# Performance work log

Measured on AMD Instinct MI355X. Metric: run time of the kernel, lower is better.

Reference implementation:

```python
import jax, jax.numpy as jnp
import numpy as np

B, C, N = 16, 128, 2048  # batch, channels (SA_Layer(128)), num points


def setup_inputs() -> dict:
    key = jax.random.key(0)
    ks = jax.random.split(key, 6)
    x = jax.random.normal(ks[0], (B, C, N), jnp.float32)
    wq = jax.random.normal(ks[1], (C // 4, C), jnp.float32) * 0.05  # shared q/k 1x1 conv, no bias
    wv = jax.random.normal(ks[2], (C, C), jnp.float32) * 0.05
    bv = jax.random.normal(ks[3], (C,), jnp.float32) * 0.05
    wt = jax.random.normal(ks[4], (C, C), jnp.float32) * 0.05
    bt = jax.random.normal(ks[5], (C,), jnp.float32) * 0.05
    gamma = jnp.ones((C,), jnp.float32)   # BatchNorm1d weight
    beta = jnp.zeros((C,), jnp.float32)   # BatchNorm1d bias
    bn_mean = jnp.zeros((C,), jnp.float32)  # running mean (eval mode)
    bn_var = jnp.ones((C,), jnp.float32)    # running var (eval mode)
    return dict(x=x, wq=wq, wv=wv, bv=bv, wt=wt, bt=bt,
                gamma=gamma, beta=beta, bn_mean=bn_mean, bn_var=bn_var)


def reference(x, wq, wv, bv, wt, bt, gamma, beta, bn_mean, bn_var):
    EPS = 1e-9
    BN_EPS = 1e-5
    # q_conv and k_conv share weights (tied in __init__)
    x_q = jnp.einsum('dc,bcn->bnd', wq, x)               # [B, N, C/4]
    x_k = jnp.einsum('dc,bcn->bdn', wq, x)               # [B, C/4, N]
    energy = jnp.einsum('bnd,bdm->bnm', x_q, x_k)        # [B, N, N]
    attn = jax.nn.softmax(energy, axis=-1)
    # offset-attention renormalization: divide by column sum
    attn = attn / (EPS + attn.sum(axis=1, keepdims=True))
    x_v = jnp.einsum('dc,bcn->bdn', wv, x) + bv[None, :, None]   # [B, C, N]
    x_r = jnp.einsum('bdn,bnm->bdm', x_v, attn)                  # [B, C, N]
    t = jnp.einsum('dc,bcn->bdn', wt, x - x_r) + bt[None, :, None]
    # BatchNorm1d (eval mode) + ReLU
    t = (t - bn_mean[None, :, None]) * jax.lax.rsqrt(bn_var + BN_EPS)[None, :, None]
    t = t * gamma[None, :, None] + beta[None, :, None]
    return x + jax.nn.relu(t)
```

## Files before the change

### kernel.cpp

```cpp
#include <hip/hip_runtime.h>
#include <hip/hip_bf16.h>
#include <math.h>

#define BB 16
#define CC 128
#define NN 2048
#define CQ 32

typedef __attribute__((ext_vector_type(8))) short bf16x8;
typedef __attribute__((ext_vector_type(4))) float f32x4;
typedef __attribute__((ext_vector_type(16))) float f32x16;

__device__ __forceinline__ ushort f2b(float f) {
    __hip_bfloat16 h = __float2bfloat16(f);
    return *reinterpret_cast<ushort*>(&h);
}
__device__ __forceinline__ float b2f(ushort u) {
    union { unsigned u; float f; } v; v.u = ((unsigned)u) << 16;
    return v.f;
}
__device__ __forceinline__ bf16x8 as_b8(uint4 u) {
    union { uint4 u; bf16x8 b; } v; v.u = u; return v.b;
}
__device__ __forceinline__ bf16x8 as_b8_2(uint2 a, uint2 b) {
    return as_b8(make_uint4(a.x, a.y, b.x, b.y));
}
__device__ __forceinline__ float fexp2(float x) {
    return __builtin_amdgcn_exp2f(x);
}

#define OFF_VB  524288
#define OFF_RSI 4718592

#define QSCALE 1.2011224087864498f

__global__ __launch_bounds__(256) void k_proj(const float* __restrict__ x,
        const float* __restrict__ wq, const float* __restrict__ wv,
        const float* __restrict__ bv, ushort* __restrict__ Qt, ushort* __restrict__ Vb) {
    __shared__ ushort Wl[160][136];
    __shared__ ushort Xs[64][136];
    int bid = (blockIdx.x & 7) * 64 + (blockIdx.x >> 3);
    int b  = bid >> 5;
    int n0 = (bid & 31) << 6;
    int tid = threadIdx.x;
    #pragma unroll
    for (int k = 0; k < 20; ++k) {
        int idx = k * 256 + tid;
        int r = idx >> 5, c4 = (idx & 31) << 2;
        const float* srcw = (r < 32) ? (wq + r * 128 + c4) : (wv + (r - 32) * 128 + c4);
        float4 w4 = *(const float4*)srcw;
        float s = (r < 32) ? QSCALE : 1.0f;
        *(ushort4*)&Wl[r][c4] = make_ushort4(f2b(w4.x * s), f2b(w4.y * s),
                                             f2b(w4.z * s), f2b(w4.w * s));
    }
    const float* xb = x + (size_t)b * CC * NN;
    for (int idx = tid; idx < 2048; idx += 256) {
        int c = idx >> 4, n4 = (idx & 15) << 2;
        float4 xv = *(const float4*)&xb[c * NN + n0 + n4];
        Xs[n4][c]     = f2b(xv.x);
        Xs[n4 + 1][c] = f2b(xv.y);
        Xs[n4 + 2][c] = f2b(xv.z);
        Xs[n4 + 3][c] = f2b(xv.w);
    }
    __syncthreads();
    int w = tid >> 6, l = tid & 63, lr = l & 15, lg = l >> 4;
    f32x4 zero = {0.f, 0.f, 0.f, 0.f};
    int nn = n0 + w * 16 + lr;
    for (int dt = 0; dt < 10; ++dt) {
        f32x4 acc = zero;
        #pragma unroll
        for (int k = 0; k < 4; ++k) {
            bf16x8 a  = *(const bf16x8*)&Wl[dt * 16 + lr][k * 32 + lg * 8];
            bf16x8 bx = *(const bf16x8*)&Xs[w * 16 + lr][k * 32 + lg * 8];
            acc = __builtin_amdgcn_mfma_f32_16x16x32_bf16(a, bx, acc, 0, 0, 0);
        }
        if (dt < 2) {
            ushort4 p = make_ushort4(f2b(acc[0]), f2b(acc[1]), f2b(acc[2]), f2b(acc[3]));
            *(ushort4*)&Qt[(size_t)(b * NN + nn) * CQ + dt * 16 + lg * 4] = p;
        } else {
            #pragma unroll
            for (int i = 0; i < 4; ++i) {
                int vd = (dt - 2) * 16 + lg * 4 + i;
                Vb[(size_t)(b * CC + vd) * NN + nn] = f2b(acc[i] + bv[vd]);
            }
        }
    }
}

__global__ __launch_bounds__(512) void k_rowstats(const ushort* __restrict__ Qt,
        float* __restrict__ RSI) {
    __shared__ ushort Qm[128][36];
    __shared__ float Sred[2][64];
    int bid = (blockIdx.x & 7) * 64 + (blockIdx.x >> 3);
    int b  = bid >> 5;
    int n0 = (bid & 31) << 6;
    int tid = threadIdx.x;
    int w = tid >> 6, l = tid & 63, lr = l & 15, lg = l >> 4;
    int wn = w & 3, wm = w >> 2;
    const ushort* Qtb = Qt + (size_t)b * NN * CQ;
    bf16x8 aq = *(const bf16x8*)&Qtb[(size_t)(n0 + wn * 16 + lr) * CQ + lg * 8];
    int sr = tid >> 2, sc = (tid & 3) * 8;
    uint4 q0 = *(const uint4*)&Qtb[(size_t)sr * CQ + sc];
    float S[4] = {0.f, 0.f, 0.f, 0.f};
    f32x4 zero = {0.f, 0.f, 0.f, 0.f};
    for (int t = 0; t < 16; ++t) {
        __syncthreads();
        *(uint4*)&Qm[sr][sc] = q0;
        __syncthreads();
        if (t < 15)
            q0 = *(const uint4*)&Qtb[(size_t)((t + 1) * 128 + sr) * CQ + sc];
        #pragma unroll
        for (int mi = 0; mi < 4; ++mi) {
            bf16x8 bq = *(const bf16x8*)&Qm[(wm * 4 + mi) * 16 + lr][lg * 8];
            f32x4 e = __builtin_amdgcn_mfma_f32_16x16x32_bf16(aq, bq, zero, 0, 0, 0);
            S[0] += fexp2(e[0]); S[1] += fexp2(e[1]);
            S[2] += fexp2(e[2]); S[3] += fexp2(e[3]);
        }
    }
    #pragma unroll
    for (int d = 1; d < 16; d <<= 1) {
        #pragma unroll
        for (int i = 0; i < 4; ++i) S[i] += __shfl_xor(S[i], d);
    }
    if (lr == 0) {
        #pragma unroll
        for (int i = 0; i < 4; ++i) Sred[wm][wn * 16 + lg * 4 + i] = S[i];
    }
    __syncthreads();
    if (tid < 64)
        RSI[b * NN + n0 + tid] = 1.f / (Sred[0][tid] + Sred[1][tid]);
}

__global__ __launch_bounds__(768, 3) void k_attn_pv(const ushort* __restrict__ Qt,
        const ushort* __restrict__ Vb, const float* __restrict__ RSI,
        const float* __restrict__ x, const float* __restrict__ wt,
        const float* __restrict__ bt, const float* __restrict__ gamma,
        const float* __restrict__ beta, const float* __restrict__ bn_mean,
        const float* __restrict__ bn_var, float* __restrict__ out) {
    __shared__ ushort Vs[2][128][68];
    __shared__ ushort Ws[2][128][68];
    __shared__ ushort wtl[16896];
    __shared__ float csred[4][128];
    __shared__ float csum[128];
    __shared__ float fAl[128], fBl[128];
    int bid = (blockIdx.x & 7) * 32 + (blockIdx.x >> 3);
    int b  = bid >> 4;
    int m0 = (bid & 15) << 7;
    int tid = threadIdx.x;
    int w = tid >> 6, l = tid & 63, lr = l & 15, lg = l >> 4;
    const ushort* Qtb = Qt + (size_t)b * NN * CQ;
    const ushort* Vbb = Vb + (size_t)b * CC * NN;
    const float*  RSb = RSI + (size_t)b * NN;
    const float*  xb  = x   + (size_t)b * CC * NN;
    float*        outb = out + (size_t)b * CC * NN;
    f32x4 zero = {0.f, 0.f, 0.f, 0.f};
    bool producer = (w < 8);

    for (int idx = tid; idx < 4096; idx += 768) {
        int r = idx >> 5, c4 = (idx & 31) << 2;
        float4 w4 = *(const float4*)&wt[r * 128 + c4];
        *(ushort4*)&wtl[r * 132 + c4] =
            make_ushort4(f2b(w4.x), f2b(w4.y), f2b(w4.z), f2b(w4.w));
    }
    if (tid < 128) {
        float A = gamma[tid] * rsqrtf(bn_var[tid] + 1e-5f);
        fAl[tid] = A;
        fBl[tid] = (bt[tid] - bn_mean[tid]) * A + beta[tid];
    }

    int wn = w & 3, mh = w >> 2;
    bf16x8 bm[4];
    float cs[4] = {0.f, 0.f, 0.f, 0.f};
    int sv = 0, shv = 0;
    const ushort* vsrc = nullptr;
    bf16x8 aq_nx; float4 rsi_nx;
    int cw = w - 8;
    int dh = cw >> 1, mh2 = cw & 1;
    int ar = l & 31, kh = l >> 5;
    f32x16 pacc00, pacc01, pacc10, pacc11;

    if (producer) {
        #pragma unroll
        for (int mi = 0; mi < 4; ++mi)
            bm[mi] = *(const bf16x8*)&Qtb[(size_t)(m0 + (mh * 4 + mi) * 16 + lr) * CQ + lg * 8];
        sv = tid >> 2; shv = (tid & 3) * 16;
        vsrc = Vbb + (size_t)sv * NN + shv;
        {
            uint4 v0 = *(const uint4*)(vsrc);
            uint4 v1 = *(const uint4*)(vsrc + 8);
            ushort* dst = &Vs[0][sv][shv];
            *(uint2*)(dst)      = make_uint2(v0.x, v0.y);
            *(uint2*)(dst + 4)  = make_uint2(v0.z, v0.w);
            *(uint2*)(dst + 8)  = make_uint2(v1.x, v1.y);
            *(uint2*)(dst + 12) = make_uint2(v1.z, v1.w);
        }
        {
            bf16x8 aq0 = *(const bf16x8*)&Qtb[(size_t)(wn * 16 + lr) * CQ + lg * 8];
            float4 r4 = *(const float4*)&RSb[wn * 16 + lg * 4];
            int nb = wn * 16 + lg * 4;
            #pragma unroll
            for (int mi = 0; mi < 4; ++mi) {
                f32x4 e = __builtin_amdgcn_mfma_f32_16x16x32_bf16(aq0, bm[mi], zero, 0, 0, 0);
                float w0 = fexp2(e[0]) * r4.x;
                float w1 = fexp2(e[1]) * r4.y;
                float w2 = fexp2(e[2]) * r4.z;
                float w3 = fexp2(e[3]) * r4.w;
                cs[mi] += w0 + w1 + w2 + w3;
                *(ushort4*)&Ws[0][(mh * 4 + mi) * 16 + lr][nb] =
                    make_ushort4(f2b(w0), f2b(w1), f2b(w2), f2b(w3));
            }
        }
        aq_nx  = *(const bf16x8*)&Qtb[(size_t)(64 + wn * 16 + lr) * CQ + lg * 8];
        rsi_nx = *(const float4*)&RSb[64 + wn * 16 + lg * 4];
    } else {
        #pragma unroll
        for (int r = 0; r < 16; ++r) {
            pacc00[r] = 0.f; pacc01[r] = 0.f; pacc10[r] = 0.f; pacc11[r] = 0.f;
        }
    }
    __syncthreads();
    for (int t = 0; t < 32; ++t) {
        int cur = t & 1;
        if (producer) {
            if (t < 31) {
                int ntn = (t + 1) * 64;
                uint4 v0 = *(const uint4*)(vsrc + ntn);
                uint4 v1 = *(const uint4*)(vsrc + ntn + 8);
                bf16x8 aq = aq_nx;
                float4 r4 = rsi_nx;
                if (t < 30) {
                    int nt2 = (t + 2) * 64;
                    aq_nx  = *(const bf16x8*)&Qtb[(size_t)(nt2 + wn * 16 + lr) * CQ + lg * 8];
                    rsi_nx = *(const float4*)&RSb[nt2 + wn * 16 + lg * 4];
                }
                int nb = wn * 16 + lg * 4;
                #pragma unroll
                for (int mi = 0; mi < 4; ++mi) {
                    f32x4 e = __builtin_amdgcn_mfma_f32_16x16x32_bf16(aq, bm[mi], zero, 0, 0, 0);
                    float w0 = fexp2(e[0]) * r4.x;
                    float w1 = fexp2(e[1]) * r4.y;
                    float w2 = fexp2(e[2]) * r4.z;
                    float w3 = fexp2(e[3]) * r4.w;
                    cs[mi] += w0 + w1 + w2 + w3;
                    *(ushort4*)&Ws[cur ^ 1][(mh * 4 + mi) * 16 + lr][nb] =
                        make_ushort4(f2b(w0), f2b(w1), f2b(w2), f2b(w3));
                }
                ushort* dst = &Vs[cur ^ 1][sv][shv];
                *(uint2*)(dst)      = make_uint2(v0.x, v0.y);
                *(uint2*)(dst + 4)  = make_uint2(v0.z, v0.w);
                *(uint2*)(dst + 8)  = make_uint2(v1.x, v1.y);
                *(uint2*)(dst + 12) = make_uint2(v1.z, v1.w);
            }
        } else {
            __builtin_amdgcn_s_setprio(1);
            #pragma unroll
            for (int kk = 0; kk < 4; ++kk) {
                const ushort* vp0 = &Vs[cur][dh * 64 + ar][kk * 16 + kh * 8];
                const ushort* vp1 = &Vs[cur][dh * 64 + 32 + ar][kk * 16 + kh * 8];
                uint2 a0 = *(const uint2*)vp0; uint2 a1 = *(const uint2*)(vp0 + 4);
                uint2 a2 = *(const uint2*)vp1; uint2 a3 = *(const uint2*)(vp1 + 4);
                bf16x8 va0 = as_b8_2(a0, a1);
                bf16x8 va1 = as_b8_2(a2, a3);
                const ushort* wp0 = &Ws[cur][mh2 * 64 + ar][kk * 16 + kh * 8];
                const ushort* wp1 = &Ws[cur][mh2 * 64 + 32 + ar][kk * 16 + kh * 8];
                uint2 b0 = *(const uint2*)wp0; uint2 b1 = *(const uint2*)(wp0 + 4);
                uint2 c0 = *(const uint2*)wp1; uint2 c1 = *(const uint2*)(wp1 + 4);
                bf16x8 wb0 = as_b8_2(b0, b1);
                bf16x8 wb1 = as_b8_2(c0, c1);
                pacc00 = __builtin_amdgcn_mfma_f32_32x32x16_bf16(va0, wb0, pacc00, 0, 0, 0);
                pacc01 = __builtin_amdgcn_mfma_f32_32x32x16_bf16(va0, wb1, pacc01, 0, 0, 0);
                pacc10 = __builtin_amdgcn_mfma_f32_32x32x16_bf16(va1, wb0, pacc10, 0, 0, 0);
                pacc11 = __builtin_amdgcn_mfma_f32_32x32x16_bf16(va1, wb1, pacc11, 0, 0, 0);
            }
            __builtin_amdgcn_s_setprio(0);
        }
        __syncthreads();
    }
    if (producer) {
        #pragma unroll
        for (int mi = 0; mi < 4; ++mi) {
            cs[mi] += __shfl_xor(cs[mi], 16);
            cs[mi] += __shfl_xor(cs[mi], 32);
        }
        if (lg == 0) {
            #pragma unroll
            for (int mi = 0; mi < 4; ++mi)
                csred[wn][(mh * 4 + mi) * 16 + lr] = cs[mi];
        }
    }
    __syncthreads();
    if (tid < 128) {
        float tot = csred[0][tid] + csred[1][tid] + csred[2][tid] + csred[3][tid];
        csum[tid] = 1.f / (1e-9f + tot);
    }
    __syncthreads();
    ushort* UsP = &Vs[0][0][0];
    if (!producer) {
        float inv0 = csum[mh2 * 64 + ar];
        float inv1 = csum[mh2 * 64 + 32 + ar];
        int mA = m0 + mh2 * 64 + ar;
        int mL = mh2 * 64 + ar;
        #pragma unroll
        for (int g = 0; g < 4; ++g) {
            int db = dh * 64 + 8 * g + 4 * kh;
            ushort4 u00, u01, u10, u11;
            #pragma unroll
            for (int j = 0; j < 4; ++j) {
                int r = 4 * g + j;
                float x00 = xb[(size_t)(db + j) * NN + mA];
                float x01 = xb[(size_t)(db + j) * NN + mA + 32];
                float x10 = xb[(size_t)(db + 32 + j) * NN + mA];
                float x11 = xb[(size_t)(db + 32 + j) * NN + mA + 32];
                ((ushort*)&u00)[j] = f2b(x00 - pacc00[r] * inv0);
                ((ushort*)&u01)[j] = f2b(x01 - pacc01[r] * inv1);
                ((ushort*)&u10)[j] = f2b(x10 - pacc10[r] * inv0);
                ((ushort*)&u11)[j] = f2b(x11 - pacc11[r] * inv1);
            }
            *(ushort4*)&UsP[mL * 132 + db]             = u00;
            *(ushort4*)&UsP[(mL + 32) * 132 + db]      = u01;
            *(ushort4*)&UsP[mL * 132 + db + 32]        = u10;
            *(ushort4*)&UsP[(mL + 32) * 132 + db + 32] = u11;
        }
    }
    __syncthreads();
    for (int tile = w; tile < 16; tile += 12) {
        int rt = tile >> 2, mt = tile & 3;
        f32x16 acc;
        #pragma unroll
        for (int r = 0; r < 16; ++r) acc[r] = 0.f;
        #pragma unroll
        for (int kk = 0; kk < 8; ++kk) {
            const ushort* ap = &wtl[(rt * 32 + ar) * 132 + kk * 16 + kh * 8];
            uint2 a0 = *(const uint2*)ap; uint2 a1 = *(const uint2*)(ap + 4);
            const ushort* bp = &UsP[(mt * 32 + ar) * 132 + kk * 16 + kh * 8];
            uint2 b0 = *(const uint2*)bp; uint2 b1 = *(const uint2*)(bp + 4);
            acc = __builtin_amdgcn_mfma_f32_32x32x16_bf16(
                as_b8_2(a0, a1), as_b8_2(b0, b1), acc, 0, 0, 0);
        }
        int m = m0 + mt * 32 + ar;
        #pragma unroll
        for (int g = 0; g < 4; ++g) {
            #pragma unroll
            for (int j = 0; j < 4; ++j) {
                int r = rt * 32 + j + 8 * g + 4 * kh;
                float t = acc[4 * g + j] * fAl[r] + fBl[r];
                t = fmaxf(t, 0.f);
                outb[(size_t)r * NN + m] = xb[(size_t)r * NN + m] + t;
            }
        }
    }
}

extern "C" void kernel_launch(void* const* d_in, const int* in_sizes, int n_in,
                              void* d_out, int out_size, void* d_ws, size_t ws_size,
                              hipStream_t stream) {
    const float* x       = (const float*)d_in[0];
    const float* wq      = (const float*)d_in[1];
    const float* wv      = (const float*)d_in[2];
    const float* bv      = (const float*)d_in[3];
    const float* wt      = (const float*)d_in[4];
    const float* bt      = (const float*)d_in[5];
    const float* gamma   = (const float*)d_in[6];
    const float* beta    = (const float*)d_in[7];
    const float* bn_mean = (const float*)d_in[8];
    const float* bn_var  = (const float*)d_in[9];
    float* out = (float*)d_out;
    float* ws  = (float*)d_ws;

    ushort* Qt   = (ushort*)ws;
    ushort* Vbp  = (ushort*)(ws + OFF_VB);
    float*  RSI  = ws + OFF_RSI;

    k_proj<<<BB * 32, 256, 0, stream>>>(x, wq, wv, bv, Qt, Vbp);
    k_rowstats<<<BB * 32, 512, 0, stream>>>(Qt, RSI);
    k_attn_pv<<<BB * 16, 768, 0, stream>>>(Qt, Vbp, RSI, x, wt, bt, gamma, beta,
                                           bn_mean, bn_var, out);
}
```

Baseline: 62.50 us.

## Quad-buffer V/W tiles, process two tiles per barrier, read wt from global

The producer/consumer loop now uses four LDS buffers and handles two 64-wide tiles per iteration, so the number of block-wide barriers drops from 32 to 16. The shared bf16 copy of wt is removed to free LDS for the extra buffers; the epilogue GEMM now loads wt as fp32 from global memory and converts it to bf16 in registers. In exchange, the producer no longer prefetches its next tile, and each consumer wave re-reads and re-converts wt from global. LDS use per block also rises, which may reduce how many blocks fit per CU.

```diff
diff --git a/kernel.cpp b/kernel.cpp
--- a/kernel.cpp
+++ b/kernel.cpp
@@ -137,9 +137,8 @@
         const float* __restrict__ bt, const float* __restrict__ gamma,
         const float* __restrict__ beta, const float* __restrict__ bn_mean,
         const float* __restrict__ bn_var, float* __restrict__ out) {
-    __shared__ ushort Vs[2][128][68];
-    __shared__ ushort Ws[2][128][68];
-    __shared__ ushort wtl[16896];
+    __shared__ ushort Vs[4][128][68];
+    __shared__ ushort Ws[4][128][68];
     __shared__ float csred[4][128];
     __shared__ float csum[128];
     __shared__ float fAl[128], fBl[128];
@@ -156,12 +155,6 @@
     f32x4 zero = {0.f, 0.f, 0.f, 0.f};
     bool producer = (w < 8);
 
-    for (int idx = tid; idx < 4096; idx += 768) {
-        int r = idx >> 5, c4 = (idx & 31) << 2;
-        float4 w4 = *(const float4*)&wt[r * 128 + c4];
-        *(ushort4*)&wtl[r * 132 + c4] =
-            make_ushort4(f2b(w4.x), f2b(w4.y), f2b(w4.z), f2b(w4.w));
-    }
     if (tid < 128) {
         float A = gamma[tid] * rsqrtf(bn_var[tid] + 1e-5f);
         fAl[tid] = A;
@@ -173,7 +166,6 @@
     float cs[4] = {0.f, 0.f, 0.f, 0.f};
     int sv = 0, shv = 0;
     const ushort* vsrc = nullptr;
-    bf16x8 aq_nx; float4 rsi_nx;
     int cw = w - 8;
     int dh = cw >> 1, mh2 = cw & 1;
     int ar = l & 31, kh = l >> 5;
@@ -185,93 +177,95 @@
             bm[mi] = *(const bf16x8*)&Qtb[(size_t)(m0 + (mh * 4 + mi) * 16 + lr) * CQ + lg * 8];
         sv = tid >> 2; shv = (tid & 3) * 16;
         vsrc = Vbb + (size_t)sv * NN + shv;
-        {
-            uint4 v0 = *(const uint4*)(vsrc);
-            uint4 v1 = *(const uint4*)(vsrc + 8);
-            ushort* dst = &Vs[0][sv][shv];
-            *(uint2*)(dst)      = make_uint2(v0.x, v0.y);
-            *(uint2*)(dst + 4)  = make_uint2(v0.z, v0.w);
-            *(uint2*)(dst + 8)  = make_uint2(v1.x, v1.y);
-            *(uint2*)(dst + 12) = make_uint2(v1.z, v1.w);
-        }
-        {
-            bf16x8 aq0 = *(const bf16x8*)&Qtb[(size_t)(wn * 16 + lr) * CQ + lg * 8];
-            float4 r4 = *(const float4*)&RSb[wn * 16 + lg * 4];
-            int nb = wn * 16 + lg * 4;
-            #pragma unroll
-            for (int mi = 0; mi < 4; ++mi) {
-                f32x4 e = __builtin_amdgcn_mfma_f32_16x16x32_bf16(aq0, bm[mi], zero, 0, 0, 0);
-                float w0 = fexp2(e[0]) * r4.x;
-                float w1 = fexp2(e[1]) * r4.y;
-                float w2 = fexp2(e[2]) * r4.z;
-                float w3 = fexp2(e[3]) * r4.w;
-                cs[mi] += w0 + w1 + w2 + w3;
-                *(ushort4*)&Ws[0][(mh * 4 + mi) * 16 + lr][nb] =
-                    make_ushort4(f2b(w0), f2b(w1), f2b(w2), f2b(w3));
-            }
-        }
-        aq_nx  = *(const bf16x8*)&Qtb[(size_t)(64 + wn * 16 + lr) * CQ + lg * 8];
-        rsi_nx = *(const float4*)&RSb[64 + wn * 16 + lg * 4];
     } else {
         #pragma unroll
         for (int r = 0; r < 16; ++r) {
             pacc00[r] = 0.f; pacc01[r] = 0.f; pacc10[r] = 0.f; pacc11[r] = 0.f;
         }
     }
-    __syncthreads();
-    for (int t = 0; t < 32; ++t) {
-        int cur = t & 1;
+
+    auto produce2 = [&](int tA) {
+        int tB = tA + 1;
+        int bqA = tA & 3, bqB = tB & 3;
+        int ntA = tA * 64, ntB = tB * 64;
+        uint4 va0 = *(const uint4*)(vsrc + ntA);
+        uint4 va1 = *(const uint4*)(vsrc + ntA + 8);
+        uint4 vb0 = *(const uint4*)(vsrc + ntB);
+        uint4 vb1 = *(const uint4*)(vsrc + ntB + 8);
+        bf16x8 aqA = *(const bf16x8*)&Qtb[(size_t)(ntA + wn * 16 + lr) * CQ + lg * 8];
+        bf16x8 aqB = *(const bf16x8*)&Qtb[(size_t)(ntB + wn * 16 + lr) * CQ + lg * 8];
+        float4 r4A = *(const float4*)&RSb[ntA + wn * 16 + lg * 4];
+        float4 r4B = *(const float4*)&RSb[ntB + wn * 16 + lg * 4];
+        int nb = wn * 16 + lg * 4;
+        #pragma unroll
+        for (int mi = 0; mi < 4; ++mi) {
+            f32x4 e = __builtin_amdgcn_mfma_f32_16x16x32_bf16(aqA, bm[mi], zero, 0, 0, 0);
+            float w0 = fexp2(e[0]) * r4A.x;
+            float w1 = fexp2(e[1]) * r4A.y;
+            float w2 = fexp2(e[2]) * r4A.z;
+            float w3 = fexp2(e[3]) * r4A.w;
+            cs[mi] += w0 + w1 + w2 + w3;
+            *(ushort4*)&Ws[bqA][(mh * 4 + mi) * 16 + lr][nb] =
+                make_ushort4(f2b(w0), f2b(w1), f2b(w2), f2b(w3));
+        }
+        {
+            ushort* dst = &Vs[bqA][sv][shv];
+            *(uint2*)(dst)      = make_uint2(va0.x, va0.y);
+            *(uint2*)(dst + 4)  = make_uint2(va0.z, va0.w);
+            *(uint2*)(dst + 8)  = make_uint2(va1.x, va1.y);
+            *(uint2*)(dst + 12) = make_uint2(va1.z, va1.w);
+        }
+        #pragma unroll
+        for (int mi = 0; mi < 4; ++mi) {
+            f32x4 e = __builtin_amdgcn_mfma_f32_16x16x32_bf16(aqB, bm[mi], zero, 0, 0, 0);
+            float w0 = fexp2(e[0]) * r4B.x;
+            float w1 = fexp2(e[1]) * r4B.y;
+            float w2 = fexp2(e[2]) * r4B.z;
+            float w3 = fexp2(e[3]) * r4B.w;
+            cs[mi] += w0 + w1 + w2 + w3;
+            *(ushort4*)&Ws[bqB][(mh * 4 + mi) * 16 + lr][nb] =
+                make_ushort4(f2b(w0), f2b(w1), f2b(w2), f2b(w3));
+        }
+        {
+            ushort* dst = &Vs[bqB][sv][shv];
+            *(uint2*)(dst)      = make_uint2(vb0.x, vb0.y);
+            *(uint2*)(dst + 4)  = make_uint2(vb0.z, vb0.w);
+            *(uint2*)(dst + 8)  = make_uint2(vb1.x, vb1.y);
+            *(uint2*)(dst + 12) = make_uint2(vb1.z, vb1.w);
+        }
+    };
+    auto consume = [&](int u) {
+        int bq = u & 3;
+        #pragma unroll
+        for (int kk = 0; kk < 4; ++kk) {
+            const ushort* vp0 = &Vs[bq][dh * 64 + ar][kk * 16 + kh * 8];
+            const ushort* vp1 = &Vs[bq][dh * 64 + 32 + ar][kk * 16 + kh * 8];
+            uint2 a0 = *(const uint2*)vp0; uint2 a1 = *(const uint2*)(vp0 + 4);
+            uint2 a2 = *(const uint2*)vp1; uint2 a3 = *(const uint2*)(vp1 + 4);
+            bf16x8 va0 = as_b8_2(a0, a1);
+            bf16x8 va1 = as_b8_2(a2, a3);
+            const ushort* wp0 = &Ws[bq][mh2 * 64 + ar][kk * 16 + kh * 8];
+            const ushort* wp1 = &Ws[bq][mh2 * 64 + 32 + ar][kk * 16 + kh * 8];
+            uint2 b0 = *(const uint2*)wp0; uint2 b1 = *(const uint2*)(wp0 + 4);
+            uint2 c0 = *(const uint2*)wp1; uint2 c1 = *(const uint2*)(wp1 + 4);
+            bf16x8 wb0 = as_b8_2(b0, b1);
+            bf16x8 wb1 = as_b8_2(c0, c1);
+            pacc00 = __builtin_amdgcn_mfma_f32_32x32x16_bf16(va0, wb0, pacc00, 0, 0, 0);
+            pacc01 = __builtin_amdgcn_mfma_f32_32x32x16_bf16(va0, wb1, pacc01, 0, 0, 0);
+            pacc10 = __builtin_amdgcn_mfma_f32_32x32x16_bf16(va1, wb0, pacc10, 0, 0, 0);
+            pacc11 = __builtin_amdgcn_mfma_f32_32x32x16_bf16(va1, wb1, pacc11, 0, 0, 0);
+        }
+    };
+
+    if (producer) produce2(0);
+    __syncthreads();
+    for (int p = 0; p < 16; ++p) {
         if (producer) {
-            if (t < 31) {
-                int ntn = (t + 1) * 64;
-                uint4 v0 = *(const uint4*)(vsrc + ntn);
-                uint4 v1 = *(const uint4*)(vsrc + ntn + 8);
-                bf16x8 aq = aq_nx;
-                float4 r4 = rsi_nx;
-                if (t < 30) {
-                    int nt2 = (t + 2) * 64;
-                    aq_nx  = *(const bf16x8*)&Qtb[(size_t)(nt2 + wn * 16 + lr) * CQ + lg * 8];
-                    rsi_nx = *(const float4*)&RSb[nt2 + wn * 16 + lg * 4];
-                }
-                int nb = wn * 16 + lg * 4;
-                #pragma unroll
-                for (int mi = 0; mi < 4; ++mi) {
-                    f32x4 e = __builtin_amdgcn_mfma_f32_16x16x32_bf16(aq, bm[mi], zero, 0, 0, 0);
-                    float w0 = fexp2(e[0]) * r4.x;
-                    float w1 = fexp2(e[1]) * r4.y;
-                    float w2 = fexp2(e[2]) * r4.z;
-                    float w3 = fexp2(e[3]) * r4.w;
-                    cs[mi] += w0 + w1 + w2 + w3;
-                    *(ushort4*)&Ws[cur ^ 1][(mh * 4 + mi) * 16 + lr][nb] =
-                        make_ushort4(f2b(w0), f2b(w1), f2b(w2), f2b(w3));
-                }
-                ushort* dst = &Vs[cur ^ 1][sv][shv];
-                *(uint2*)(dst)      = make_uint2(v0.x, v0.y);
-                *(uint2*)(dst + 4)  = make_uint2(v0.z, v0.w);
-                *(uint2*)(dst + 8)  = make_uint2(v1.x, v1.y);
-                *(uint2*)(dst + 12) = make_uint2(v1.z, v1.w);
-            }
+            if (p < 15) produce2(2 * p + 2);
         } else {
             __builtin_amdgcn_s_setprio(1);
-            #pragma unroll
-            for (int kk = 0; kk < 4; ++kk) {
-                const ushort* vp0 = &Vs[cur][dh * 64 + ar][kk * 16 + kh * 8];
-                const ushort* vp1 = &Vs[cur][dh * 64 + 32 + ar][kk * 16 + kh * 8];
-                uint2 a0 = *(const uint2*)vp0; uint2 a1 = *(const uint2*)(vp0 + 4);
-                uint2 a2 = *(const uint2*)vp1; uint2 a3 = *(const uint2*)(vp1 + 4);
-                bf16x8 va0 = as_b8_2(a0, a1);
-                bf16x8 va1 = as_b8_2(a2, a3);
-                const ushort* wp0 = &Ws[cur][mh2 * 64 + ar][kk * 16 + kh * 8];
-                const ushort* wp1 = &Ws[cur][mh2 * 64 + 32 + ar][kk * 16 + kh * 8];
-                uint2 b0 = *(const uint2*)wp0; uint2 b1 = *(const uint2*)(wp0 + 4);
-                uint2 c0 = *(const uint2*)wp1; uint2 c1 = *(const uint2*)(wp1 + 4);
-                bf16x8 wb0 = as_b8_2(b0, b1);
-                bf16x8 wb1 = as_b8_2(c0, c1);
-                pacc00 = __builtin_amdgcn_mfma_f32_32x32x16_bf16(va0, wb0, pacc00, 0, 0, 0);
-                pacc01 = __builtin_amdgcn_mfma_f32_32x32x16_bf16(va0, wb1, pacc01, 0, 0, 0);
-                pacc10 = __builtin_amdgcn_mfma_f32_32x32x16_bf16(va1, wb0, pacc10, 0, 0, 0);
-                pacc11 = __builtin_amdgcn_mfma_f32_32x32x16_bf16(va1, wb1, pacc11, 0, 0, 0);
-            }
+            consume(2 * p);
+            consume(2 * p + 1);
             __builtin_amdgcn_s_setprio(0);
         }
         __syncthreads();
@@ -330,12 +324,18 @@
         for (int r = 0; r < 16; ++r) acc[r] = 0.f;
         #pragma unroll
         for (int kk = 0; kk < 8; ++kk) {
-            const ushort* ap = &wtl[(rt * 32 + ar) * 132 + kk * 16 + kh * 8];
-            uint2 a0 = *(const uint2*)ap; uint2 a1 = *(const uint2*)(ap + 4);
+            const float* ap = &wt[(rt * 32 + ar) * 128 + kk * 16 + kh * 8];
+            float4 wa = *(const float4*)ap;
+            float4 wb4 = *(const float4*)(ap + 4);
+            union { ushort u[8]; bf16x8 v; } af;
+            af.u[0] = f2b(wa.x);  af.u[1] = f2b(wa.y);
+            af.u[2] = f2b(wa.z);  af.u[3] = f2b(wa.w);
+            af.u[4] = f2b(wb4.x); af.u[5] = f2b(wb4.y);
+            af.u[6] = f2b(wb4.z); af.u[7] = f2b(wb4.w);
             const ushort* bp = &UsP[(mt * 32 + ar) * 132 + kk * 16 + kh * 8];
             uint2 b0 = *(const uint2*)bp; uint2 b1 = *(const uint2*)(bp + 4);
             acc = __builtin_amdgcn_mfma_f32_32x32x16_bf16(
-                as_b8_2(a0, a1), as_b8_2(b0, b1), acc, 0, 0, 0);
+                af.v, as_b8_2(b0, b1), acc, 0, 0, 0);
         }
         int m = m0 + mt * 32 + ar;
         #pragma unroll
```

Result: slower. 68.75 us (+10.0%).

## Switch attention-value product to FP8 e4m3 MFMA with scaled weights

Applied to the files above, without the earlier changes.

Stores the V projection and the normalized attention weights as FP8 e4m3 instead of bf16, and runs the PV product with 32x32x16 fp8 MFMA. Row-sum inverses are scaled by 256 so the weights sit in FP8's usable range, and the column-sum epsilon is rescaled to match. This halves the LDS footprint, LDS read traffic and V global reads in the main attention loop. The cost is reduced precision on the attention output, which may exceed the tolerance.

```diff
diff --git a/kernel.cpp b/kernel.cpp
--- a/kernel.cpp
+++ b/kernel.cpp
@@ -1,5 +1,6 @@
 #include <hip/hip_runtime.h>
 #include <hip/hip_bf16.h>
+#include <hip/hip_fp8.h>
 #include <math.h>
 
 #define BB 16
@@ -10,6 +11,7 @@
 typedef __attribute__((ext_vector_type(8))) short bf16x8;
 typedef __attribute__((ext_vector_type(4))) float f32x4;
 typedef __attribute__((ext_vector_type(16))) float f32x16;
+typedef unsigned char uchar;
 
 __device__ __forceinline__ ushort f2b(float f) {
     __hip_bfloat16 h = __float2bfloat16(f);
@@ -19,6 +21,10 @@
     union { unsigned u; float f; } v; v.u = ((unsigned)u) << 16;
     return v.f;
 }
+__device__ __forceinline__ uchar f2q(float f) {
+    __hip_fp8_e4m3 q(f);
+    return *reinterpret_cast<uchar*>(&q);
+}
 __device__ __forceinline__ bf16x8 as_b8(uint4 u) {
     union { uint4 u; bf16x8 b; } v; v.u = u; return v.b;
 }
@@ -28,6 +34,7 @@
 __device__ __forceinline__ float fexp2(float x) {
     return __builtin_amdgcn_exp2f(x);
 }
+union U2L { uint2 u; long l; };
 
 #define OFF_VB  524288
 #define OFF_RSI 4718592
@@ -36,7 +43,7 @@
 
 __global__ __launch_bounds__(256) void k_proj(const float* __restrict__ x,
         const float* __restrict__ wq, const float* __restrict__ wv,
-        const float* __restrict__ bv, ushort* __restrict__ Qt, ushort* __restrict__ Vb) {
+        const float* __restrict__ bv, ushort* __restrict__ Qt, uchar* __restrict__ Vb) {
     __shared__ ushort Wl[160][136];
     __shared__ ushort Xs[64][136];
     int bid = (blockIdx.x & 7) * 64 + (blockIdx.x >> 3);
@@ -81,7 +88,7 @@
             #pragma unroll
             for (int i = 0; i < 4; ++i) {
                 int vd = (dt - 2) * 16 + lg * 4 + i;
-                Vb[(size_t)(b * CC + vd) * NN + nn] = f2b(acc[i] + bv[vd]);
+                Vb[(size_t)(b * CC + vd) * NN + nn] = f2q(acc[i] + bv[vd]);
             }
         }
     }
@@ -128,17 +135,16 @@
     }
     __syncthreads();
     if (tid < 64)
-        RSI[b * NN + n0 + tid] = 1.f / (Sred[0][tid] + Sred[1][tid]);
+        RSI[b * NN + n0 + tid] = 256.f / (Sred[0][tid] + Sred[1][tid]);
 }
 
 __global__ __launch_bounds__(768, 3) void k_attn_pv(const ushort* __restrict__ Qt,
-        const ushort* __restrict__ Vb, const float* __restrict__ RSI,
+        const uchar* __restrict__ Vb, const float* __restrict__ RSI,
         const float* __restrict__ x, const float* __restrict__ wt,
         const float* __restrict__ bt, const float* __restrict__ gamma,
         const float* __restrict__ beta, const float* __restrict__ bn_mean,
         const float* __restrict__ bn_var, float* __restrict__ out) {
-    __shared__ ushort Vs[2][128][68];
-    __shared__ ushort Ws[2][128][68];
+    __shared__ uchar SMp[2][2][128][72];
     __shared__ ushort wtl[16896];
     __shared__ float csred[4][128];
     __shared__ float csum[128];
@@ -149,7 +155,7 @@
     int tid = threadIdx.x;
     int w = tid >> 6, l = tid & 63, lr = l & 15, lg = l >> 4;
     const ushort* Qtb = Qt + (size_t)b * NN * CQ;
-    const ushort* Vbb = Vb + (size_t)b * CC * NN;
+    const uchar*  Vbb = Vb + (size_t)b * CC * NN;
     const float*  RSb = RSI + (size_t)b * NN;
     const float*  xb  = x   + (size_t)b * CC * NN;
     float*        outb = out + (size_t)b * CC * NN;
@@ -172,7 +178,7 @@
     bf16x8 bm[4];
     float cs[4] = {0.f, 0.f, 0.f, 0.f};
     int sv = 0, shv = 0;
-    const ushort* vsrc = nullptr;
+    const uchar* vsrc = nullptr;
     bf16x8 aq_nx; float4 rsi_nx;
     int cw = w - 8;
     int dh = cw >> 1, mh2 = cw & 1;
@@ -187,12 +193,9 @@
         vsrc = Vbb + (size_t)sv * NN + shv;
         {
             uint4 v0 = *(const uint4*)(vsrc);
-            uint4 v1 = *(const uint4*)(vsrc + 8);
-            ushort* dst = &Vs[0][sv][shv];
-            *(uint2*)(dst)      = make_uint2(v0.x, v0.y);
-            *(uint2*)(dst + 4)  = make_uint2(v0.z, v0.w);
-            *(uint2*)(dst + 8)  = make_uint2(v1.x, v1.y);
-            *(uint2*)(dst + 12) = make_uint2(v1.z, v1.w);
+            uchar* dst = &SMp[0][0][sv][shv];
+            *(uint2*)(dst)     = make_uint2(v0.x, v0.y);
+            *(uint2*)(dst + 8) = make_uint2(v0.z, v0.w);
         }
         {
             bf16x8 aq0 = *(const bf16x8*)&Qtb[(size_t)(wn * 16 + lr) * CQ + lg * 8];
@@ -206,8 +209,10 @@
                 float w2 = fexp2(e[2]) * r4.z;
                 float w3 = fexp2(e[3]) * r4.w;
                 cs[mi] += w0 + w1 + w2 + w3;
-                *(ushort4*)&Ws[0][(mh * 4 + mi) * 16 + lr][nb] =
-                    make_ushort4(f2b(w0), f2b(w1), f2b(w2), f2b(w3));
+                union { uchar b[4]; uint u; } pw;
+                pw.b[0] = f2q(w0); pw.b[1] = f2q(w1);
+                pw.b[2] = f2q(w2); pw.b[3] = f2q(w3);
+                *(uint*)&SMp[1][0][(mh * 4 + mi) * 16 + lr][nb] = pw.u;
             }
         }
         aq_nx  = *(const bf16x8*)&Qtb[(size_t)(64 + wn * 16 + lr) * CQ + lg * 8];
@@ -225,7 +230,6 @@
             if (t < 31) {
                 int ntn = (t + 1) * 64;
                 uint4 v0 = *(const uint4*)(vsrc + ntn);
-                uint4 v1 = *(const uint4*)(vsrc + ntn + 8);
                 bf16x8 aq = aq_nx;
                 float4 r4 = rsi_nx;
                 if (t < 30) {
@@ -242,35 +246,29 @@
                     float w2 = fexp2(e[2]) * r4.z;
                     float w3 = fexp2(e[3]) * r4.w;
                     cs[mi] += w0 + w1 + w2 + w3;
-                    *(ushort4*)&Ws[cur ^ 1][(mh * 4 + mi) * 16 + lr][nb] =
-                        make_ushort4(f2b(w0), f2b(w1), f2b(w2), f2b(w3));
+                    union { uchar b[4]; uint u; } pw;
+                    pw.b[0] = f2q(w0); pw.b[1] = f2q(w1);
+                    pw.b[2] = f2q(w2); pw.b[3] = f2q(w3);
+                    *(uint*)&SMp[1][cur ^ 1][(mh * 4 + mi) * 16 + lr][nb] = pw.u;
                 }
-                ushort* dst = &Vs[cur ^ 1][sv][shv];
-                *(uint2*)(dst)      = make_uint2(v0.x, v0.y);
-                *(uint2*)(dst + 4)  = make_uint2(v0.z, v0.w);
-                *(uint2*)(dst + 8)  = make_uint2(v1.x, v1.y);
-                *(uint2*)(dst + 12) = make_uint2(v1.z, v1.w);
+                uchar* dst = &SMp[0][cur ^ 1][sv][shv];
+                *(uint2*)(dst)     = make_uint2(v0.x, v0.y);
+                *(uint2*)(dst + 8) = make_uint2(v0.z, v0.w);
             }
         } else {
             __builtin_amdgcn_s_setprio(1);
             #pragma unroll
             for (int kk = 0; kk < 4; ++kk) {
-                const ushort* vp0 = &Vs[cur][dh * 64 + ar][kk * 16 + kh * 8];
-                const ushort* vp1 = &Vs[cur][dh * 64 + 32 + ar][kk * 16 + kh * 8];
-                uint2 a0 = *(const uint2*)vp0; uint2 a1 = *(const uint2*)(vp0 + 4);
-                uint2 a2 = *(const uint2*)vp1; uint2 a3 = *(const uint2*)(vp1 + 4);
-                bf16x8 va0 = as_b8_2(a0, a1);
-                bf16x8 va1 = as_b8_2(a2, a3);
-                const ushort* wp0 = &Ws[cur][mh2 * 64 + ar][kk * 16 + kh * 8];
-                const ushort* wp1 = &Ws[cur][mh2 * 64 + 32 + ar][kk * 16 + kh * 8];
-                uint2 b0 = *(const uint2*)wp0; uint2 b1 = *(const uint2*)(wp0 + 4);
-                uint2 c0 = *(const uint2*)wp1; uint2 c1 = *(const uint2*)(wp1 + 4);
-                bf16x8 wb0 = as_b8_2(b0, b1);
-                bf16x8 wb1 = as_b8_2(c0, c1);
-                pacc00 = __builtin_amdgcn_mfma_f32_32x32x16_bf16(va0, wb0, pacc00, 0, 0, 0);
-                pacc01 = __builtin_amdgcn_mfma_f32_32x32x16_bf16(va0, wb1, pacc01, 0, 0, 0);
-                pacc10 = __builtin_amdgcn_mfma_f32_32x32x16_bf16(va1, wb0, pacc10, 0, 0, 0);
-                pacc11 = __builtin_amdgcn_mfma_f32_32x32x16_bf16(va1, wb1, pacc11, 0, 0, 0);
+                int cb = kk * 16 + kh * 8;
+                U2L va0, va1, wb0, wb1;
+                va0.u = *(const uint2*)&SMp[0][cur][dh * 64 + ar][cb];
+                va1.u = *(const uint2*)&SMp[0][cur][dh * 64 + 32 + ar][cb];
+                wb0.u = *(const uint2*)&SMp[1][cur][mh2 * 64 + ar][cb];
+                wb1.u = *(const uint2*)&SMp[1][cur][mh2 * 64 + 32 + ar][cb];
+                pacc00 = __builtin_amdgcn_mfma_f32_32x32x16_fp8_fp8(va0.l, wb0.l, pacc00, 0, 0, 0);
+                pacc01 = __builtin_amdgcn_mfma_f32_32x32x16_fp8_fp8(va0.l, wb1.l, pacc01, 0, 0, 0);
+                pacc10 = __builtin_amdgcn_mfma_f32_32x32x16_fp8_fp8(va1.l, wb0.l, pacc10, 0, 0, 0);
+                pacc11 = __builtin_amdgcn_mfma_f32_32x32x16_fp8_fp8(va1.l, wb1.l, pacc11, 0, 0, 0);
             }
             __builtin_amdgcn_s_setprio(0);
         }
@@ -291,10 +289,10 @@
     __syncthreads();
     if (tid < 128) {
         float tot = csred[0][tid] + csred[1][tid] + csred[2][tid] + csred[3][tid];
-        csum[tid] = 1.f / (1e-9f + tot);
-    }
-    __syncthreads();
-    ushort* UsP = &Vs[0][0][0];
+        csum[tid] = 1.f / (2.56e-7f + tot);
+    }
+    __syncthreads();
+    ushort* UsP = (ushort*)&SMp[0][0][0][0];
     if (!producer) {
         float inv0 = csum[mh2 * 64 + ar];
         float inv1 = csum[mh2 * 64 + 32 + ar];
@@ -368,7 +366,7 @@
     float* ws  = (float*)d_ws;
 
     ushort* Qt   = (ushort*)ws;
-    ushort* Vbp  = (ushort*)(ws + OFF_VB);
+    uchar*  Vbp  = (uchar*)(ws + OFF_VB);
     float*  RSI  = ws + OFF_RSI;
 
     k_proj<<<BB * 32, 256, 0, stream>>>(x, wq, wv, bv, Qt, Vbp);
```

Measured after the change: 66.99 us. 1.07x slower.
